# Optimization experiments

Measured on AMD Instinct MI355X. Metric: run time of the kernel, lower is better.

## Reference

```python
import jax, jax.numpy as jnp
import numpy as np

N, E, H, C, IN = 50000, 500000, 4, 64, 256


def setup_inputs() -> dict:
    key = jax.random.key(0)
    ks = jax.random.split(key, 16)
    sW = 1.0 / np.sqrt(IN)
    sA = 1.0 / np.sqrt(C)
    inp = {
        "x": jax.random.normal(ks[0], (N, IN), jnp.float32),
        "edge_index": jax.random.randint(ks[1], (2, E), 0, N, jnp.int64 if jax.config.jax_enable_x64 else jnp.int32),
        "W1": jax.random.normal(ks[2], (IN, H * C), jnp.float32) * sW,
        "as1": jax.random.normal(ks[3], (H, C), jnp.float32) * sA,
        "ad1": jax.random.normal(ks[4], (H, C), jnp.float32) * sA,
        "b1": jnp.zeros((H * C,), jnp.float32),
        "W2": jax.random.normal(ks[5], (H * C, H * C), jnp.float32) * sW,
        "as2": jax.random.normal(ks[6], (H, C), jnp.float32) * sA,
        "ad2": jax.random.normal(ks[7], (H, C), jnp.float32) * sA,
        "b2": jnp.zeros((H * C,), jnp.float32),
        "WN": jax.random.normal(ks[8], (H * C, H * C), jnp.float32) * sW,
        "asN": jax.random.normal(ks[9], (H, C), jnp.float32) * sA,
        "adN": jax.random.normal(ks[10], (H, C), jnp.float32) * sA,
        "bN": jnp.zeros((H * C,), jnp.float32),
    }
    return inp


def _gat_conv(x, src, dst, W, a_src, a_dst, b, n_nodes):
    # x: [N, F_in]; src/dst: [E'] (self-loops included); W: [F_in, H*C]
    Hh, Cc = a_src.shape
    h = (x @ W).reshape(n_nodes, Hh, Cc)                      # [N,H,C]
    e_src = jnp.einsum("nhc,hc->nh", h, a_src)                # [N,H]
    e_dst = jnp.einsum("nhc,hc->nh", h, a_dst)
    e = jax.nn.leaky_relu(e_src[src] + e_dst[dst], 0.2)       # [E',H]
    m = jax.lax.stop_gradient(jax.ops.segment_max(e, dst, num_segments=n_nodes))
    ex = jnp.exp(e - m[dst])
    denom = jax.ops.segment_sum(ex, dst, num_segments=n_nodes)
    alpha = ex / (denom[dst] + 1e-16)                         # [E',H]
    out = jax.ops.segment_sum(h[src] * alpha[:, :, None], dst, num_segments=n_nodes)
    return out.reshape(n_nodes, Hh * Cc) + b


def reference(x, edge_index, W1, as1, ad1, b1, W2, as2, ad2, b2, WN, asN, adN, bN):
    n = x.shape[0]
    loops = jnp.arange(n, dtype=edge_index.dtype)
    src = jnp.concatenate([edge_index[0], loops])  # PyG GATConv add_self_loops=True
    dst = jnp.concatenate([edge_index[1], loops])
    inp = x
    h = jax.nn.relu(_gat_conv(x, src, dst, W1, as1, ad1, b1, n)) + inp
    h = jax.nn.relu(_gat_conv(h, src, dst, W2, as2, ad2, b2, n))
    h = _gat_conv(h, src, dst, WN, asN, adN, bN, n)
    # eval mode: F.dropout is identity
    return jax.nn.relu(h + inp)
```

## Files before the change

### kernel.cpp

```cpp
#include <hip/hip_runtime.h>
#include <hip/hip_bf16.h>
#include <math.h>

typedef short short8 __attribute__((ext_vector_type(8)));
typedef float f32x4 __attribute__((ext_vector_type(4)));

static __device__ __forceinline__ float bfu(unsigned short u) {
    union { unsigned int i; float f; } c; c.i = ((unsigned int)u) << 16; return c.f;
}


__global__ void k_cast_bf16(const float* __restrict__ in, __hip_bfloat16* __restrict__ out, int n) {
    int i4 = (blockIdx.x * blockDim.x + threadIdx.x) * 4;
    if (i4 >= n) return;
    float4 f = *(const float4*)(in + i4);
    union { ushort u[4]; uint2 v; } o;
    __hip_bfloat16 h0 = __float2bfloat16(f.x); o.u[0] = *(ushort*)&h0;
    __hip_bfloat16 h1 = __float2bfloat16(f.y); o.u[1] = *(ushort*)&h1;
    __hip_bfloat16 h2 = __float2bfloat16(f.z); o.u[2] = *(ushort*)&h2;
    __hip_bfloat16 h3 = __float2bfloat16(f.w); o.u[3] = *(ushort*)&h3;
    *(uint2*)(out + i4) = o.v;
}

__global__ void k_wt_cast(const float* __restrict__ W, __hip_bfloat16* __restrict__ Wt) {
    int n = blockIdx.x, k = threadIdx.x;
    Wt[n * 256 + k] = __float2bfloat16(W[k * 256 + n]);
}


__global__ void k_set1(int* a, int n) {
    int i = blockIdx.x * blockDim.x + threadIdx.x;
    if (i < n) a[i] = 1;
}

__global__ void k_hist(const int* __restrict__ dstv, int* __restrict__ cnt, int E) {
    int i = blockIdx.x * blockDim.x + threadIdx.x;
    if (i < E) atomicAdd(&cnt[dstv[i]], 1);
}

__global__ void k_scan1(const int* __restrict__ cnt, int* __restrict__ excl, int* __restrict__ bsum, int n) {
    __shared__ int s[256];
    int i = blockIdx.x * 256 + threadIdx.x;
    int v = (i < n) ? cnt[i] : 0;
    s[threadIdx.x] = v;
    __syncthreads();
    for (int off = 1; off < 256; off <<= 1) {
        int t = (threadIdx.x >= off) ? s[threadIdx.x - off] : 0;
        __syncthreads();
        s[threadIdx.x] += t;
        __syncthreads();
    }
    if (i < n) excl[i] = s[threadIdx.x] - v;
    if (threadIdx.x == 255) bsum[blockIdx.x] = s[255];
}

__global__ void k_scan2(const int* __restrict__ bsum, int* __restrict__ boff, int nb) {
    __shared__ int s[256];
    int carry = 0;
    for (int base = 0; base < nb; base += 256) {
        int i = base + threadIdx.x;
        int v = (i < nb) ? bsum[i] : 0;
        s[threadIdx.x] = v;
        __syncthreads();
        for (int off = 1; off < 256; off <<= 1) {
            int t = (threadIdx.x >= off) ? s[threadIdx.x - off] : 0;
            __syncthreads();
            s[threadIdx.x] += t;
            __syncthreads();
        }
        if (i < nb) boff[i] = carry + s[threadIdx.x] - v;
        carry += s[255];
        __syncthreads();
    }
}

__global__ void k_scan3(const int* __restrict__ excl, const int* __restrict__ boff,
                        int* __restrict__ rowptr, int* __restrict__ cursor, int n, int Etot) {
    int i = blockIdx.x * blockDim.x + threadIdx.x;
    if (i < n) {
        int v = excl[i] + boff[i >> 8];
        rowptr[i] = v;
        cursor[i] = v;
    }
    if (i == 0) rowptr[n] = Etot;
}

__global__ void k_scatter(const int* __restrict__ srcv, const int* __restrict__ dstv,
                          int* __restrict__ cursor, int* __restrict__ colsrc, int E, int Nn) {
    int i = blockIdx.x * blockDim.x + threadIdx.x;
    if (i < E) {
        int pos = atomicAdd(&cursor[dstv[i]], 1);
        colsrc[pos] = srcv[i];
    } else if (i < E + Nn) {
        int nn = i - E;
        int pos = atomicAdd(&cursor[nn], 1);
        colsrc[pos] = nn;
    }
}


__global__ __launch_bounds__(256) void k_gemm(const __hip_bfloat16* __restrict__ A,
                                              const __hip_bfloat16* __restrict__ Wt,
                                              __hip_bfloat16* __restrict__ C,
                                              const float* __restrict__ a_src,
                                              const float* __restrict__ a_dst,
                                              float* __restrict__ es,
                                              float* __restrict__ ed, int M) {
    __shared__ __align__(16) char As[128 * 128];
    __shared__ __align__(16) char Bs[256 * 128];
    int tid = threadIdx.x;
    int w = tid >> 6, l = tid & 63;
    int m0 = blockIdx.x * 128;
    f32x4 acc[8][4];
#pragma unroll
    for (int a = 0; a < 8; ++a)
#pragma unroll
        for (int b = 0; b < 4; ++b) acc[a][b] = (f32x4){0.f, 0.f, 0.f, 0.f};

    for (int bk = 0; bk < 256; bk += 64) {
        __syncthreads();
#pragma unroll
        for (int i = 0; i < 4; ++i) {
            int c = tid + 256 * i;
            int row = c >> 3, ko = c & 7;
            int rg = m0 + row;
            uint4 v = {0u, 0u, 0u, 0u};
            if (rg < M) v = *(const uint4*)((const char*)A + (size_t)rg * 512 + bk * 2 + ko * 16);
            int off = (ko * 16) ^ ((row & 7) << 4);
            *(uint4*)(As + row * 128 + off) = v;
        }
#pragma unroll
        for (int i = 0; i < 8; ++i) {
            int c = tid + 256 * i;
            int row = c >> 3, ko = c & 7;
            uint4 v = *(const uint4*)((const char*)Wt + (size_t)row * 512 + bk * 2 + ko * 16);
            int off = (ko * 16) ^ ((row & 7) << 4);
            *(uint4*)(Bs + row * 128 + off) = v;
        }
        __syncthreads();
        int lo = l & 15, hi = l >> 4;
#pragma unroll
        for (int kk = 0; kk < 2; ++kk) {
            int koff = kk * 64 + hi * 16;
            short8 bfr[4];
#pragma unroll
            for (int ni = 0; ni < 4; ++ni) {
                int row = w * 64 + ni * 16 + lo;
                bfr[ni] = *(const short8*)(Bs + row * 128 + (koff ^ ((row & 7) << 4)));
            }
#pragma unroll
            for (int mi = 0; mi < 8; ++mi) {
                int row = mi * 16 + lo;
                short8 af = *(const short8*)(As + row * 128 + (koff ^ ((row & 7) << 4)));
#pragma unroll
                for (int ni = 0; ni < 4; ++ni)
                    acc[mi][ni] = __builtin_amdgcn_mfma_f32_16x16x32_bf16(af, bfr[ni], acc[mi][ni], 0, 0, 0);
            }
        }
    }
    int lo = l & 15, hi = l >> 4;
#pragma unroll
    for (int mi = 0; mi < 8; ++mi) {
#pragma unroll
        for (int r = 0; r < 4; ++r) {
            int rg = m0 + mi * 16 + hi * 4 + r;
            if (rg < M) {
#pragma unroll
                for (int ni = 0; ni < 4; ++ni) {
                    int col = w * 64 + ni * 16 + lo;
                    C[(size_t)rg * 256 + col] = __float2bfloat16(acc[mi][ni][r]);
                }
            }
        }
    }
    float avv[4], adv[4];
#pragma unroll
    for (int ni = 0; ni < 4; ++ni) {
        avv[ni] = a_src[w * 64 + ni * 16 + lo];
        adv[ni] = a_dst[w * 64 + ni * 16 + lo];
    }
#pragma unroll
    for (int mi = 0; mi < 8; ++mi) {
#pragma unroll
        for (int r = 0; r < 4; ++r) {
            int rg = m0 + mi * 16 + hi * 4 + r;
            float s1 = 0.f, s2 = 0.f;
#pragma unroll
            for (int ni = 0; ni < 4; ++ni) {
                s1 += acc[mi][ni][r] * avv[ni];
                s2 += acc[mi][ni][r] * adv[ni];
            }
#pragma unroll
            for (int mk = 1; mk < 16; mk <<= 1) {
                s1 += __shfl_xor(s1, mk, 64);
                s2 += __shfl_xor(s2, mk, 64);
            }
            if (lo == 0 && rg < M) {
                es[rg * 4 + w] = s1;
                ed[rg * 4 + w] = s2;
            }
        }
    }
}


__global__ __launch_bounds__(256) void k_aggregate(const __hip_bfloat16* __restrict__ hW,
                            const int* __restrict__ rowptr,
                            const int* __restrict__ colsrc, const float* __restrict__ es,
                            const float* __restrict__ edv_, const float* __restrict__ bias,
                            const float* __restrict__ xres, __hip_bfloat16* __restrict__ outbf,
                            float* __restrict__ outf, int mode, int Nn) {
    int n = blockIdx.x * 4 + (threadIdx.x >> 6);
    if (n >= Nn) return;
    int l = threadIdx.x & 63;
    int h = l >> 4;
    int r0 = rowptr[n];
    int deg = rowptr[n + 1] - r0;
    float edv = edv_[n * 4 + h];

    float denom = 0.f;
    float a0 = 0.f, a1 = 0.f, a2 = 0.f, a3 = 0.f;
    const ushort* hw = (const ushort*)hW;
    int sfb = colsrc[r0];

    for (int base = 0; base < deg; base += 8) {
        int sv[8];
#pragma unroll
        for (int u = 0; u < 8; ++u)
            sv[u] = (base + u < deg) ? colsrc[r0 + base + u] : sfb;
        float ev[8];
#pragma unroll
        for (int u = 0; u < 8; ++u)
            ev[u] = es[(size_t)sv[u] * 4 + h];
        uint2 hv[8];
#pragma unroll
        for (int u = 0; u < 8; ++u)
            hv[u] = *(const uint2*)(hw + (size_t)sv[u] * 256 + l * 4);
#pragma unroll
        for (int u = 0; u < 8; ++u) {
            float t = ev[u] + edv;
            t = fmaxf(t, 0.2f * t);
            float p = (base + u < deg) ? __expf(t) : 0.f;
            denom += p;
            a0 += p * bfu((ushort)(hv[u].x & 0xffff));
            a1 += p * bfu((ushort)(hv[u].x >> 16));
            a2 += p * bfu((ushort)(hv[u].y & 0xffff));
            a3 += p * bfu((ushort)(hv[u].y >> 16));
        }
    }

    float inv = 1.f / (denom + 1e-16f);
    int idx = n * 256 + l * 4;
    float4 b4 = *(const float4*)(bias + l * 4);
    float v0 = a0 * inv + b4.x;
    float v1 = a1 * inv + b4.y;
    float v2 = a2 * inv + b4.z;
    float v3 = a3 * inv + b4.w;

    if (mode == 2) {
        float4 x4 = *(const float4*)(xres + idx);
        float4 o;
        o.x = fmaxf(v0 + x4.x, 0.f);
        o.y = fmaxf(v1 + x4.y, 0.f);
        o.z = fmaxf(v2 + x4.z, 0.f);
        o.w = fmaxf(v3 + x4.w, 0.f);
        *(float4*)(outf + idx) = o;
    } else {
        v0 = fmaxf(v0, 0.f); v1 = fmaxf(v1, 0.f);
        v2 = fmaxf(v2, 0.f); v3 = fmaxf(v3, 0.f);
        if (mode == 0) {
            float4 x4 = *(const float4*)(xres + idx);
            v0 += x4.x; v1 += x4.y; v2 += x4.z; v3 += x4.w;
        }
        union { ushort u[4]; uint2 v; } o;
        __hip_bfloat16 h0 = __float2bfloat16(v0); o.u[0] = *(ushort*)&h0;
        __hip_bfloat16 h1 = __float2bfloat16(v1); o.u[1] = *(ushort*)&h1;
        __hip_bfloat16 h2 = __float2bfloat16(v2); o.u[2] = *(ushort*)&h2;
        __hip_bfloat16 h3 = __float2bfloat16(v3); o.u[3] = *(ushort*)&h3;
        *(uint2*)((ushort*)outbf + idx) = o.v;
    }
}


extern "C" void kernel_launch(void* const* d_in, const int* in_sizes, int n_in,
                              void* d_out, int out_size, void* d_ws, size_t ws_size,
                              hipStream_t stream) {
    const float* x  = (const float*)d_in[0];
    const int* ei   = (const int*)d_in[1];
    const float* W1 = (const float*)d_in[2];
    const float* as1 = (const float*)d_in[3];
    const float* ad1 = (const float*)d_in[4];
    const float* b1  = (const float*)d_in[5];
    const float* W2  = (const float*)d_in[6];
    const float* as2 = (const float*)d_in[7];
    const float* ad2 = (const float*)d_in[8];
    const float* b2  = (const float*)d_in[9];
    const float* WN  = (const float*)d_in[10];
    const float* asN = (const float*)d_in[11];
    const float* adN = (const float*)d_in[12];
    const float* bN  = (const float*)d_in[13];

    int Nn = in_sizes[0] / 256;
    int E = in_sizes[1] / 2;
    const int* srcv = ei;
    const int* dstv = ei + E;
    int Etot = E + Nn;

    char* p = (char*)d_ws;
    auto alloc = [&](size_t bytes) {
        char* r = p;
        p += (bytes + 255) & ~(size_t)255;
        return r;
    };
    __hip_bfloat16* xbf  = (__hip_bfloat16*)alloc((size_t)Nn * 256 * 2);
    __hip_bfloat16* Pbf  = (__hip_bfloat16*)alloc((size_t)Nn * 256 * 2);
    __hip_bfloat16* Qbf  = (__hip_bfloat16*)alloc((size_t)Nn * 256 * 2);
    __hip_bfloat16* hWbf = (__hip_bfloat16*)alloc((size_t)Nn * 256 * 2);
    __hip_bfloat16* Wt1  = (__hip_bfloat16*)alloc(256 * 256 * 2);
    __hip_bfloat16* Wt2  = (__hip_bfloat16*)alloc(256 * 256 * 2);
    __hip_bfloat16* Wt3  = (__hip_bfloat16*)alloc(256 * 256 * 2);
    float* esrc = (float*)alloc((size_t)Nn * 4 * 4);
    float* edst = (float*)alloc((size_t)Nn * 4 * 4);
    int* cnt    = (int*)alloc((size_t)Nn * 4);
    int* excl   = (int*)alloc((size_t)Nn * 4);
    int* rowptr = (int*)alloc((size_t)(Nn + 1) * 4);
    int* cursor = (int*)alloc((size_t)Nn * 4);
    int* bsum   = (int*)alloc(4096);
    int* boff   = (int*)alloc(4096);
    int* colsrc = (int*)alloc((size_t)Etot * 4);

    int nb = (Nn + 255) / 256;

    k_cast_bf16<<<(Nn * 256 / 4 + 255) / 256, 256, 0, stream>>>(x, xbf, Nn * 256);
    k_wt_cast<<<256, 256, 0, stream>>>(W1, Wt1);
    k_wt_cast<<<256, 256, 0, stream>>>(W2, Wt2);
    k_wt_cast<<<256, 256, 0, stream>>>(WN, Wt3);

    k_set1<<<nb, 256, 0, stream>>>(cnt, Nn);
    k_hist<<<(E + 255) / 256, 256, 0, stream>>>(dstv, cnt, E);
    k_scan1<<<nb, 256, 0, stream>>>(cnt, excl, bsum, Nn);
    k_scan2<<<1, 256, 0, stream>>>(bsum, boff, nb);
    k_scan3<<<nb, 256, 0, stream>>>(excl, boff, rowptr, cursor, Nn, Etot);
    k_scatter<<<(Etot + 255) / 256, 256, 0, stream>>>(srcv, dstv, cursor, colsrc, E, Nn);

    int gg = (Nn + 127) / 128;
    int ga = (Nn + 3) / 4;

    k_gemm<<<gg, 256, 0, stream>>>(xbf, Wt1, hWbf, as1, ad1, esrc, edst, Nn);
    k_aggregate<<<ga, 256, 0, stream>>>(hWbf, rowptr, colsrc, esrc, edst, b1, x, Pbf, nullptr, 0, Nn);
    k_gemm<<<gg, 256, 0, stream>>>(Pbf, Wt2, hWbf, as2, ad2, esrc, edst, Nn);
    k_aggregate<<<ga, 256, 0, stream>>>(hWbf, rowptr, colsrc, esrc, edst, b2, x, Qbf, nullptr, 1, Nn);
    k_gemm<<<gg, 256, 0, stream>>>(Qbf, Wt3, hWbf, asN, adN, esrc, edst, Nn);
    k_aggregate<<<ga, 256, 0, stream>>>(hWbf, rowptr, colsrc, esrc, edst, bN, x, nullptr, (float*)d_out, 2, Nn);
}
```

Measured before the change: 348.2 us.

## Fuse x bf16 cast into first GEMM, halve GEMM M-tile, merge weight casts

Removes the standalone fp32-to-bf16 cast of x. The first GEMM now loads fp32 rows directly and converts them while staging into shared memory, which saves one full pass over x (read plus a bf16 write). The GEMM row tile shrinks from 128 to 64, doubling the block count to about 782 and cutting accumulator registers and LDS, which aims for better occupancy across the many CUs. The three weight-transpose casts are merged into a single launch. The tradeoff is that each block reloads the full B tile for fewer rows, so weight traffic from L2 goes up.

```diff
diff --git a/kernel.cpp b/kernel.cpp
--- a/kernel.cpp
+++ b/kernel.cpp
@@ -8,22 +8,18 @@
 static __device__ __forceinline__ float bfu(unsigned short u) {
     union { unsigned int i; float f; } c; c.i = ((unsigned int)u) << 16; return c.f;
 }
-
-
-__global__ void k_cast_bf16(const float* __restrict__ in, __hip_bfloat16* __restrict__ out, int n) {
-    int i4 = (blockIdx.x * blockDim.x + threadIdx.x) * 4;
-    if (i4 >= n) return;
-    float4 f = *(const float4*)(in + i4);
-    union { ushort u[4]; uint2 v; } o;
-    __hip_bfloat16 h0 = __float2bfloat16(f.x); o.u[0] = *(ushort*)&h0;
-    __hip_bfloat16 h1 = __float2bfloat16(f.y); o.u[1] = *(ushort*)&h1;
-    __hip_bfloat16 h2 = __float2bfloat16(f.z); o.u[2] = *(ushort*)&h2;
-    __hip_bfloat16 h3 = __float2bfloat16(f.w); o.u[3] = *(ushort*)&h3;
-    *(uint2*)(out + i4) = o.v;
-}
-
-__global__ void k_wt_cast(const float* __restrict__ W, __hip_bfloat16* __restrict__ Wt) {
+static __device__ __forceinline__ ushort f2bu(float f) {
+    __hip_bfloat16 h = __float2bfloat16(f);
+    return *(ushort*)&h;
+}
+
+
+__global__ void k_wt_cast3(const float* __restrict__ W1, const float* __restrict__ W2,
+                           const float* __restrict__ W3, __hip_bfloat16* __restrict__ Wt1,
+                           __hip_bfloat16* __restrict__ Wt2, __hip_bfloat16* __restrict__ Wt3) {
     int n = blockIdx.x, k = threadIdx.x;
+    const float* W = (blockIdx.y == 0) ? W1 : (blockIdx.y == 1) ? W2 : W3;
+    __hip_bfloat16* Wt = (blockIdx.y == 0) ? Wt1 : (blockIdx.y == 1) ? Wt2 : Wt3;
     Wt[n * 256 + k] = __float2bfloat16(W[k * 256 + n]);
 }
 
@@ -99,33 +95,46 @@
 }
 
 
-__global__ __launch_bounds__(256) void k_gemm(const __hip_bfloat16* __restrict__ A,
+template <bool AFP32>
+__global__ __launch_bounds__(256) void k_gemm(const void* __restrict__ Ap,
                                               const __hip_bfloat16* __restrict__ Wt,
                                               __hip_bfloat16* __restrict__ C,
                                               const float* __restrict__ a_src,
                                               const float* __restrict__ a_dst,
                                               float* __restrict__ es,
                                               float* __restrict__ ed, int M) {
-    __shared__ __align__(16) char As[128 * 128];
+    __shared__ __align__(16) char As[64 * 128];
     __shared__ __align__(16) char Bs[256 * 128];
     int tid = threadIdx.x;
     int w = tid >> 6, l = tid & 63;
-    int m0 = blockIdx.x * 128;
-    f32x4 acc[8][4];
-#pragma unroll
-    for (int a = 0; a < 8; ++a)
+    int m0 = blockIdx.x * 64;
+    f32x4 acc[4][4];
+#pragma unroll
+    for (int a = 0; a < 4; ++a)
 #pragma unroll
         for (int b = 0; b < 4; ++b) acc[a][b] = (f32x4){0.f, 0.f, 0.f, 0.f};
 
     for (int bk = 0; bk < 256; bk += 64) {
         __syncthreads();
 #pragma unroll
-        for (int i = 0; i < 4; ++i) {
+        for (int i = 0; i < 2; ++i) {
             int c = tid + 256 * i;
             int row = c >> 3, ko = c & 7;
             int rg = m0 + row;
             uint4 v = {0u, 0u, 0u, 0u};
-            if (rg < M) v = *(const uint4*)((const char*)A + (size_t)rg * 512 + bk * 2 + ko * 16);
+            if (rg < M) {
+                if (AFP32) {
+                    const float* Af = (const float*)Ap;
+                    float4 f0 = *(const float4*)(Af + (size_t)rg * 256 + bk + ko * 8);
+                    float4 f1 = *(const float4*)(Af + (size_t)rg * 256 + bk + ko * 8 + 4);
+                    v.x = (uint)f2bu(f0.x) | ((uint)f2bu(f0.y) << 16);
+                    v.y = (uint)f2bu(f0.z) | ((uint)f2bu(f0.w) << 16);
+                    v.z = (uint)f2bu(f1.x) | ((uint)f2bu(f1.y) << 16);
+                    v.w = (uint)f2bu(f1.z) | ((uint)f2bu(f1.w) << 16);
+                } else {
+                    v = *(const uint4*)((const char*)Ap + (size_t)rg * 512 + bk * 2 + ko * 16);
+                }
+            }
             int off = (ko * 16) ^ ((row & 7) << 4);
             *(uint4*)(As + row * 128 + off) = v;
         }
@@ -142,25 +151,27 @@
 #pragma unroll
         for (int kk = 0; kk < 2; ++kk) {
             int koff = kk * 64 + hi * 16;
-            short8 bfr[4];
+            short8 af[4], bfr[4];
+#pragma unroll
+            for (int mi = 0; mi < 4; ++mi) {
+                int row = mi * 16 + lo;
+                af[mi] = *(const short8*)(As + row * 128 + (koff ^ ((row & 7) << 4)));
+            }
 #pragma unroll
             for (int ni = 0; ni < 4; ++ni) {
                 int row = w * 64 + ni * 16 + lo;
                 bfr[ni] = *(const short8*)(Bs + row * 128 + (koff ^ ((row & 7) << 4)));
             }
 #pragma unroll
-            for (int mi = 0; mi < 8; ++mi) {
-                int row = mi * 16 + lo;
-                short8 af = *(const short8*)(As + row * 128 + (koff ^ ((row & 7) << 4)));
+            for (int mi = 0; mi < 4; ++mi)
 #pragma unroll
                 for (int ni = 0; ni < 4; ++ni)
-                    acc[mi][ni] = __builtin_amdgcn_mfma_f32_16x16x32_bf16(af, bfr[ni], acc[mi][ni], 0, 0, 0);
-            }
+                    acc[mi][ni] = __builtin_amdgcn_mfma_f32_16x16x32_bf16(af[mi], bfr[ni], acc[mi][ni], 0, 0, 0);
         }
     }
     int lo = l & 15, hi = l >> 4;
 #pragma unroll
-    for (int mi = 0; mi < 8; ++mi) {
+    for (int mi = 0; mi < 4; ++mi) {
 #pragma unroll
         for (int r = 0; r < 4; ++r) {
             int rg = m0 + mi * 16 + hi * 4 + r;
@@ -180,7 +191,7 @@
         adv[ni] = a_dst[w * 64 + ni * 16 + lo];
     }
 #pragma unroll
-    for (int mi = 0; mi < 8; ++mi) {
+    for (int mi = 0; mi < 4; ++mi) {
 #pragma unroll
         for (int r = 0; r < 4; ++r) {
             int rg = m0 + mi * 16 + hi * 4 + r;
@@ -273,10 +284,8 @@
             v0 += x4.x; v1 += x4.y; v2 += x4.z; v3 += x4.w;
         }
         union { ushort u[4]; uint2 v; } o;
-        __hip_bfloat16 h0 = __float2bfloat16(v0); o.u[0] = *(ushort*)&h0;
-        __hip_bfloat16 h1 = __float2bfloat16(v1); o.u[1] = *(ushort*)&h1;
-        __hip_bfloat16 h2 = __float2bfloat16(v2); o.u[2] = *(ushort*)&h2;
-        __hip_bfloat16 h3 = __float2bfloat16(v3); o.u[3] = *(ushort*)&h3;
+        o.u[0] = f2bu(v0); o.u[1] = f2bu(v1);
+        o.u[2] = f2bu(v2); o.u[3] = f2bu(v3);
         *(uint2*)((ushort*)outbf + idx) = o.v;
     }
 }
@@ -312,7 +321,6 @@
         p += (bytes + 255) & ~(size_t)255;
         return r;
     };
-    __hip_bfloat16* xbf  = (__hip_bfloat16*)alloc((size_t)Nn * 256 * 2);
     __hip_bfloat16* Pbf  = (__hip_bfloat16*)alloc((size_t)Nn * 256 * 2);
     __hip_bfloat16* Qbf  = (__hip_bfloat16*)alloc((size_t)Nn * 256 * 2);
     __hip_bfloat16* hWbf = (__hip_bfloat16*)alloc((size_t)Nn * 256 * 2);
@@ -331,10 +339,8 @@
 
     int nb = (Nn + 255) / 256;
 
-    k_cast_bf16<<<(Nn * 256 / 4 + 255) / 256, 256, 0, stream>>>(x, xbf, Nn * 256);
-    k_wt_cast<<<256, 256, 0, stream>>>(W1, Wt1);
-    k_wt_cast<<<256, 256, 0, stream>>>(W2, Wt2);
-    k_wt_cast<<<256, 256, 0, stream>>>(WN, Wt3);
+    dim3 wg(256, 3);
+    k_wt_cast3<<<wg, 256, 0, stream>>>(W1, W2, WN, Wt1, Wt2, Wt3);
 
     k_set1<<<nb, 256, 0, stream>>>(cnt, Nn);
     k_hist<<<(E + 255) / 256, 256, 0, stream>>>(dstv, cnt, E);
@@ -343,13 +349,13 @@
     k_scan3<<<nb, 256, 0, stream>>>(excl, boff, rowptr, cursor, Nn, Etot);
     k_scatter<<<(Etot + 255) / 256, 256, 0, stream>>>(srcv, dstv, cursor, colsrc, E, Nn);
 
-    int gg = (Nn + 127) / 128;
+    int gg = (Nn + 63) / 64;
     int ga = (Nn + 3) / 4;
 
-    k_gemm<<<gg, 256, 0, stream>>>(xbf, Wt1, hWbf, as1, ad1, esrc, edst, Nn);
+    k_gemm<true><<<gg, 256, 0, stream>>>(x, Wt1, hWbf, as1, ad1, esrc, edst, Nn);
     k_aggregate<<<ga, 256, 0, stream>>>(hWbf, rowptr, colsrc, esrc, edst, b1, x, Pbf, nullptr, 0, Nn);
-    k_gemm<<<gg, 256, 0, stream>>>(Pbf, Wt2, hWbf, as2, ad2, esrc, edst, Nn);
+    k_gemm<false><<<gg, 256, 0, stream>>>(Pbf, Wt2, hWbf, as2, ad2, esrc, edst, Nn);
     k_aggregate<<<ga, 256, 0, stream>>>(hWbf, rowptr, colsrc, esrc, edst, b2, x, Qbf, nullptr, 1, Nn);
-    k_gemm<<<gg, 256, 0, stream>>>(Qbf, Wt3, hWbf, asN, adN, esrc, edst, Nn);
+    k_gemm<false><<<gg, 256, 0, stream>>>(Qbf, Wt3, hWbf, asN, adN, esrc, edst, Nn);
     k_aggregate<<<ga, 256, 0, stream>>>(hWbf, rowptr, colsrc, esrc, edst, bN, x, nullptr, (float*)d_out, 2, Nn);
 }
```

After: 300.3 us. 13.8% less time.
